# Performance work log

Hardware: AMD Instinct MI355X
Metric: run time of the kernel (lower is better)

Reference implementation:

```python
import jax, jax.numpy as jnp
import numpy as np

N = 50000      # nodes
E = 800000     # edges (avg degree 16)
F_IN = 128
HID = 64
NCLS = 40
K = 2          # num_stacks
T = 2          # num_layers (shared weights)


def setup_inputs() -> dict:
    key = jax.random.key(0)
    ks = jax.random.split(key, 10)
    s = 0.05
    return {
        "x": jax.random.normal(ks[0], (N, F_IN), dtype=jnp.float32),
        "edge_index": jax.random.randint(ks[1], (2, E), 0, N),
        "w1_init": jax.random.normal(ks[2], (K, F_IN, HID), dtype=jnp.float32) * s,
        "w1": jax.random.normal(ks[3], (K, HID, HID), dtype=jnp.float32) * s,
        "v1": jax.random.normal(ks[4], (K, F_IN, HID), dtype=jnp.float32) * s,
        "b1": jax.random.normal(ks[5], (K, HID), dtype=jnp.float32) * s,
        "w2_init": jax.random.normal(ks[6], (K, HID, NCLS), dtype=jnp.float32) * s,
        "w2": jax.random.normal(ks[7], (K, NCLS, NCLS), dtype=jnp.float32) * s,
        "v2": jax.random.normal(ks[8], (K, HID, NCLS), dtype=jnp.float32) * s,
        "b2": jax.random.normal(ks[9], (K, NCLS), dtype=jnp.float32) * s,
    }


def _gcn_norm(src, dst, n):
    # PyG gcn_norm with add_self_loops=False: deg over destination, sym norm
    deg = jax.ops.segment_sum(jnp.ones_like(dst, dtype=jnp.float32), dst, num_segments=n)
    dinv = jnp.where(deg > 0, 1.0 / jnp.sqrt(deg), 0.0)
    return dinv[src] * dinv[dst]  # [E]


def _arma_conv(x, src, dst, norm, n, w_init, w, v, b, act):
    # x: [N, Fin]; w_init: [K, Fin, Fout]; w: [K, Fout, Fout]; v: [K, Fin, Fout]; b: [K, Fout]
    root = jnp.einsum('nf,kfg->kng', x, v)  # [K, N, Fout], dropout=0 -> identity
    out = None
    for t in range(T):
        if t == 0:
            h = jnp.einsum('nf,kfg->kng', x, w_init)
        else:
            h = jnp.einsum('knf,kfg->kng', out, w)
        # sparse neighbor aggregation: out[i] = sum_{(j->i)} norm_e * h[j]
        agg = jax.vmap(
            lambda hk: jax.ops.segment_sum(hk[src] * norm[:, None], dst, num_segments=n)
        )(h)  # [K, N, Fout]
        out = act(agg + root + b[:, None, :])
    return out.mean(axis=0)  # mean over stacks -> [N, Fout]


def reference(x, edge_index, w1_init, w1, v1, b1, w2_init, w2, v2, b2):
    src, dst = edge_index[0], edge_index[1]
    norm = _gcn_norm(src, dst, N)
    h = _arma_conv(x, src, dst, norm, N, w1_init, w1, v1, b1, jax.nn.relu)
    h = jax.nn.relu(h)  # wrapper ReLU; dropout is identity in eval
    o = _arma_conv(h, src, dst, norm, N, w2_init, w2, v2, b2, lambda z: z)
    return jax.nn.log_softmax(o, axis=1)
```

## Files before the change

kernel.cpp:

```cpp
#include <hip/hip_runtime.h>
#include <hip/hip_bf16.h>
#include <math.h>

#define N_NODES 50000
#define F_IN 128
#define HID 64
#define NCLS 40
#define K_STACKS 2
#define SCAN_TILE 1024
#define NBLK_CNT 256

typedef __attribute__((ext_vector_type(8))) short short8;
typedef __attribute__((ext_vector_type(4))) float floatx4;

__device__ __forceinline__ unsigned int f32_to_bf16_bits(float f) {
    unsigned int u = __float_as_uint(f);
    return (u + 0x7fffu + ((u >> 16) & 1u)) >> 16;
}
__device__ __forceinline__ unsigned int pack_bf16x2(float a, float b) {
    return f32_to_bf16_bits(a) | (f32_to_bf16_bits(b) << 16);
}


__global__ __launch_bounds__(256) void count_kernel(const int* __restrict__ dst,
                                                    int* __restrict__ counts, int E) {
    __shared__ int hist[256];
    int blk = blockIdx.x, t = threadIdx.x;
    hist[t] = 0;
    __syncthreads();
    int chunk = (E + NBLK_CNT - 1) / NBLK_CNT;
    int s = blk * chunk, e = min(E, s + chunk);
    for (int i = s + t; i < e; i += 256) atomicAdd(&hist[dst[i] >> 8], 1);
    __syncthreads();
    counts[t * NBLK_CNT + blk] = hist[t];
}

__global__ __launch_bounds__(256) void scan_phase1(const int* __restrict__ in,
                                                   int* __restrict__ blockSums, int n) {
    __shared__ int lds[256];
    int b = blockIdx.x, t = threadIdx.x;
    int base = b * SCAN_TILE + t * 4;
    int s = 0;
    if (base + 3 < n) {
        int4 v = *(const int4*)(in + base);
        s = v.x + v.y + v.z + v.w;
    } else {
#pragma unroll
        for (int i = 0; i < 4; ++i)
            if (base + i < n) s += in[base + i];
    }
    lds[t] = s;
    __syncthreads();
    for (int off = 128; off; off >>= 1) {
        if (t < off) lds[t] += lds[t + off];
        __syncthreads();
    }
    if (t == 0) blockSums[b] = lds[0];
}

__global__ void scan_phase2(int* __restrict__ blockSums, int nb) {
    int t = threadIdx.x;
    int v = (t < nb) ? blockSums[t] : 0;
#pragma unroll
    for (int off = 1; off < 64; off <<= 1) {
        int u = __shfl_up(v, off);
        if (t >= off) v += u;
    }
    if (t < nb) blockSums[t] = v;
}

__global__ __launch_bounds__(256) void scan_phase3_excl(const int* __restrict__ in,
                                                        const int* __restrict__ blockSumsInc,
                                                        int* __restrict__ out, int n) {
    __shared__ int lds[256];
    int b = blockIdx.x, t = threadIdx.x;
    int base = b * SCAN_TILE + t * 4;
    int e[4];
    int s = 0;
#pragma unroll
    for (int i = 0; i < 4; ++i) {
        e[i] = (base + i < n) ? in[base + i] : 0;
        s += e[i];
    }
    lds[t] = s;
    __syncthreads();
    int v = s;
    for (int off = 1; off < 256; off <<= 1) {
        int add = (t >= off) ? lds[t - off] : 0;
        __syncthreads();
        v += add;
        lds[t] = v;
        __syncthreads();
    }
    int run = (t == 0 ? 0 : lds[t - 1]) + (b == 0 ? 0 : blockSumsInc[b - 1]);
#pragma unroll
    for (int i = 0; i < 4; ++i) {
        if (base + i < n) {
            out[base + i] = run;
            run += e[i];
        }
    }
}

__global__ __launch_bounds__(256) void bucket_scatter_kernel(const int* __restrict__ src,
                                                             const int* __restrict__ dst,
                                                             const int* __restrict__ scanned,
                                                             unsigned int* __restrict__ pairs,
                                                             int E) {
    __shared__ int cur[256];
    int blk = blockIdx.x, t = threadIdx.x;
    cur[t] = scanned[t * NBLK_CNT + blk];
    __syncthreads();
    int chunk = (E + NBLK_CNT - 1) / NBLK_CNT;
    int s0 = blk * chunk, e0 = min(E, s0 + chunk);
    for (int i = s0 + t; i < e0; i += 256) {
        int d = dst[i];
        int pos = atomicAdd(&cur[d >> 8], 1);
        pairs[pos] = (unsigned int)src[i] | ((unsigned int)(d & 255) << 16);
    }
}

__global__ __launch_bounds__(256) void csr_build_kernel(const unsigned int* __restrict__ pairs,
                                                        const int* __restrict__ scanned,
                                                        int* __restrict__ row_ptr,
                                                        float* __restrict__ dinv,
                                                        int* __restrict__ col, int N, int E) {
    __shared__ int degl[256], lds[256], curl[256], sb[2];
    int b = blockIdx.x, t = threadIdx.x;
    if (t == 0) {
        sb[0] = scanned[b * NBLK_CNT];
        sb[1] = (b + 1 < 256) ? scanned[(b + 1) * NBLK_CNT] : E;
    }
    degl[t] = 0;
    __syncthreads();
    int bstart = sb[0], bend = sb[1];
    for (int e = bstart + t; e < bend; e += 256) {
        atomicAdd(&degl[(pairs[e] >> 16) & 255], 1);
    }
    __syncthreads();
    int d = degl[t];
    lds[t] = d;
    __syncthreads();
    int v = d;
    for (int off = 1; off < 256; off <<= 1) {
        int add = (t >= off) ? lds[t - off] : 0;
        __syncthreads();
        v += add;
        lds[t] = v;
        __syncthreads();
    }
    int excl = v - d;
    int node = b * 256 + t;
    if (node <= N) row_ptr[node] = bstart + excl;
    if (node < N) dinv[node] = (d > 0) ? (1.0f / sqrtf((float)d)) : 0.0f;
    curl[t] = excl;
    __syncthreads();
    for (int e = bstart + t; e < bend; e += 256) {
        unsigned int p = pairs[e];
        int ln = (p >> 16) & 255;
        int pos = atomicAdd(&curl[ln], 1);
        col[bstart + pos] = (int)(p & 0xffffu);
    }
}

__device__ __forceinline__ void wt_one(const float* __restrict__ in,
                                       unsigned short* __restrict__ out, int li, int C, int F,
                                       int CP) {
    int k = li / (F * CP);
    int r = li - k * F * CP;
    int f = r / CP;
    int c = r - f * CP;
    out[li] = (c < C) ? (unsigned short)f32_to_bf16_bits(in[((size_t)k * C + c) * F + f]) : 0;
}

__global__ void wt_all_kernel(const float* v1, const float* w1i, const float* w1,
                              const float* v2, const float* w2i, const float* w2,
                              unsigned short* v1t, unsigned short* w1it, unsigned short* w1t,
                              unsigned short* v2t, unsigned short* w2it, unsigned short* w2t) {
    int i = blockIdx.x * blockDim.x + threadIdx.x;
    if (i < 16384) wt_one(v1, v1t, i, 128, 64, 128);
    else if (i < 32768) wt_one(w1i, w1it, i - 16384, 128, 64, 128);
    else if (i < 40960) wt_one(w1, w1t, i - 32768, 64, 64, 64);
    else if (i < 46080) wt_one(v2, v2t, i - 40960, 64, 40, 64);
    else if (i < 51200) wt_one(w2i, w2it, i - 46080, 64, 40, 64);
    else if (i < 56320) wt_one(w2, w2t, i - 51200, 40, 40, 64);
}

template <int CINP>
__global__ __launch_bounds__(256) void gemm_mfma(
    const void* __restrict__ A, const unsigned short* __restrict__ Bt,
    void* __restrict__ out, const float* __restrict__ scale, int N, int COUT, int CREAL,
    int a_per_k, int a_bf16, int out_bf16, int do_scale, int out_inter) {
    constexpr int CP8 = CINP / 8;
    constexpr int MS = CP8 - 1;
    constexpr int SH = (CP8 == 16) ? 4 : 3;
    __shared__ __align__(16) unsigned short At[64 * CINP];
    __shared__ __align__(16) unsigned short Bs[64 * CINP];

    const int k = blockIdx.y;
    const int n0 = blockIdx.x * 64;
    const int t = threadIdx.x;
    const size_t abase = a_per_k ? (size_t)k * N * CREAL : (size_t)0;
    const unsigned short* Bk = Bt + (size_t)k * COUT * CINP;

    for (int i = t; i < 64 * CP8; i += 256) {
        int n = i >> SH;
        int c = i & MS;
        uint4 w = make_uint4(0u, 0u, 0u, 0u);
        int gn = n0 + n;
        if (gn < N && c * 8 < CREAL) {
            if (a_bf16) {
                w = *(const uint4*)((const unsigned short*)A + abase + (size_t)gn * CREAL + c * 8);
            } else {
                const float* srcp = (const float*)A + abase + (size_t)gn * CREAL + c * 8;
                float4 f0 = *(const float4*)(srcp);
                float4 f1 = *(const float4*)(srcp + 4);
                w.x = pack_bf16x2(f0.x, f0.y);
                w.y = pack_bf16x2(f0.z, f0.w);
                w.z = pack_bf16x2(f1.x, f1.y);
                w.w = pack_bf16x2(f1.z, f1.w);
            }
        }
        *(uint4*)(At + n * CINP + ((c ^ (n & MS)) << 3)) = w;
    }
    for (int i = t; i < COUT * CP8; i += 256) {
        int f = i >> SH;
        int c = i & MS;
        uint4 w = *(const uint4*)(Bk + f * CINP + c * 8);
        *(uint4*)(Bs + f * CINP + ((c ^ (f & MS)) << 3)) = w;
    }
    __syncthreads();

    const int lane = t & 63;
    const int wv = t >> 6;
    const int quad = lane >> 4;
    const int li = lane & 15;
    const int m0 = wv * 16;

    floatx4 acc[4] = {{0.f, 0.f, 0.f, 0.f}, {0.f, 0.f, 0.f, 0.f},
                      {0.f, 0.f, 0.f, 0.f}, {0.f, 0.f, 0.f, 0.f}};
    const int am = (m0 + li) & MS;
#pragma unroll
    for (int kc = 0; kc < CINP / 32; ++kc) {
        int cc = kc * 4 + quad;
        short8 a = *(const short8*)(At + (m0 + li) * CINP + ((cc ^ am) << 3));
#pragma unroll
        for (int nt = 0; nt < 4; ++nt) {
            if (nt * 16 < COUT) {
                int f = nt * 16 + li;
                short8 b = *(const short8*)(Bs + f * CINP + ((cc ^ (f & MS)) << 3));
                acc[nt] = __builtin_amdgcn_mfma_f32_16x16x32_bf16(a, b, acc[nt], 0, 0, 0);
            }
        }
    }

    float sc[4] = {1.f, 1.f, 1.f, 1.f};
    if (do_scale) {
#pragma unroll
        for (int r = 0; r < 4; ++r) {
            int node = n0 + m0 + quad * 4 + r;
            sc[r] = (node < N) ? scale[node] : 1.f;
        }
    }
#pragma unroll
    for (int nt = 0; nt < 4; ++nt) {
        if (nt * 16 >= COUT) continue;
        int f = nt * 16 + li;
        if (f >= COUT) continue;
#pragma unroll
        for (int r = 0; r < 4; ++r) {
            int node = n0 + m0 + quad * 4 + r;
            if (node < N) {
                size_t o = out_inter ? ((size_t)node * 2 * COUT + (size_t)k * COUT + f)
                                     : (((size_t)k * N + node) * COUT + f);
                float val = acc[nt][r] * sc[r];
                if (out_bf16)
                    ((unsigned short*)out)[o] = (unsigned short)f32_to_bf16_bits(val);
                else
                    ((float*)out)[o] = val;
            }
        }
    }
}

template <int F>
__global__ __launch_bounds__(256) void agg_kernel(
    const unsigned short* __restrict__ h, const int* __restrict__ row_ptr,
    const int* __restrict__ col, const float* __restrict__ dinv,
    const unsigned short* __restrict__ rootb, const float* __restrict__ bias,
    void* __restrict__ out, int N, int do_relu, int out_bf16) {
    constexpr int FH = F / 8;
    constexpr int ROWE = 2 * F;
    int wid = (blockIdx.x * blockDim.x + threadIdx.x) >> 6;
    int lane = threadIdx.x & 63;
    int node = wid;
    if (node >= N) return;
    int e0 = row_ptr[node];
    int deg = row_ptr[node + 1] - e0;
    float dv = dinv[node];
    const int sub = lane >> 4;
    const int fq = lane & 15;
    const int kk = fq >> 3;
    const int fqq = fq & 7;
    const int fqc = (fqq < FH) ? fqq : (FH - 1);
    const int foff = kk * F + fqc * 8;

    float acc[8] = {};
    for (int w0 = 0; w0 < deg; w0 += 64) {
        int mye = w0 + lane;
        int c = (mye < deg) ? col[e0 + mye] : 0;
        int nch = min(deg - w0, 64);
        for (int base = 0; base < nch; base += 16) {
            uint4 v[4];
            float wj[4];
#pragma unroll
            for (int u = 0; u < 4; ++u) {
                int j = base + u * 4 + sub;
                int cj = __shfl(c, j);
                bool ok = (j < nch);
                wj[u] = ok ? 1.f : 0.f;
                int cs = ok ? cj : 0;
                v[u] = *(const uint4*)(h + (size_t)cs * ROWE + foff);
            }
#pragma unroll
            for (int u = 0; u < 4; ++u) {
                const unsigned int uu[4] = {v[u].x, v[u].y, v[u].z, v[u].w};
#pragma unroll
                for (int q = 0; q < 4; ++q) {
                    float lo = __uint_as_float(uu[q] << 16);
                    float hi = __uint_as_float(uu[q] & 0xffff0000u);
                    acc[2 * q] += wj[u] * lo;
                    acc[2 * q + 1] += wj[u] * hi;
                }
            }
        }
    }
#pragma unroll
    for (int m = 16; m < 64; m <<= 1) {
#pragma unroll
        for (int i = 0; i < 8; ++i) acc[i] += __shfl_xor(acc[i], m);
    }
    if (sub == 0 && fqq < FH) {
        size_t o = ((size_t)kk * N + node) * F + fqq * 8;
        uint4 rv = *(const uint4*)(rootb + o);
        const float* bp = bias + kk * F + fqq * 8;
        float4 b0 = *(const float4*)(bp);
        float4 b1 = *(const float4*)(bp + 4);
        const unsigned int ru[4] = {rv.x, rv.y, rv.z, rv.w};
        float r[8];
#pragma unroll
        for (int q = 0; q < 4; ++q) {
            r[2 * q] = __uint_as_float(ru[q] << 16);
            r[2 * q + 1] = __uint_as_float(ru[q] & 0xffff0000u);
        }
        float res[8] = {acc[0] * dv + r[0] + b0.x, acc[1] * dv + r[1] + b0.y,
                        acc[2] * dv + r[2] + b0.z, acc[3] * dv + r[3] + b0.w,
                        acc[4] * dv + r[4] + b1.x, acc[5] * dv + r[5] + b1.y,
                        acc[6] * dv + r[6] + b1.z, acc[7] * dv + r[7] + b1.w};
        if (do_relu) {
#pragma unroll
            for (int i = 0; i < 8; ++i) res[i] = fmaxf(res[i], 0.f);
        }
        if (out_bf16) {
            uint4 w;
            w.x = pack_bf16x2(res[0], res[1]);
            w.y = pack_bf16x2(res[2], res[3]);
            w.z = pack_bf16x2(res[4], res[5]);
            w.w = pack_bf16x2(res[6], res[7]);
            *(uint4*)((unsigned short*)out + o) = w;
        } else {
            *(float4*)((float*)out + o) = make_float4(res[0], res[1], res[2], res[3]);
            *(float4*)((float*)out + o + 4) = make_float4(res[4], res[5], res[6], res[7]);
        }
    }
}

__global__ void mean_relu_kernel(const float* __restrict__ in, float* __restrict__ out,
                                 size_t cnt, size_t stride) {
    size_t i = (size_t)blockIdx.x * blockDim.x + threadIdx.x;
    if (i < cnt) out[i] = fmaxf(0.5f * (in[i] + in[i + stride]), 0.f);
}

__global__ __launch_bounds__(256) void lsm_kernel(const float* __restrict__ g,
                                                  float* __restrict__ out, int N) {
    int wid = (blockIdx.x * blockDim.x + threadIdx.x) >> 6;
    int lane = threadIdx.x & 63;
    if (wid >= N) return;
    float v = -INFINITY;
    if (lane < NCLS)
        v = 0.5f * (g[(size_t)wid * NCLS + lane] + g[((size_t)N + wid) * NCLS + lane]);
    float m = v;
#pragma unroll
    for (int off = 32; off; off >>= 1) m = fmaxf(m, __shfl_xor(m, off));
    float ex = (lane < NCLS) ? expf(v - m) : 0.f;
    float s = ex;
#pragma unroll
    for (int off = 32; off; off >>= 1) s += __shfl_xor(s, off);
    float r = v - m - logf(s);
    if (lane < NCLS) out[(size_t)wid * NCLS + lane] = r;
}


static inline size_t align256(size_t x) { return (x + 255) & ~(size_t)255; }

extern "C" void kernel_launch(void* const* d_in, const int* in_sizes, int n_in,
                              void* d_out, int out_size, void* d_ws, size_t ws_size,
                              hipStream_t stream) {
    const float* x = (const float*)d_in[0];
    const int* ei = (const int*)d_in[1];
    const float* w1_init = (const float*)d_in[2];
    const float* w1 = (const float*)d_in[3];
    const float* v1 = (const float*)d_in[4];
    const float* b1 = (const float*)d_in[5];
    const float* w2_init = (const float*)d_in[6];
    const float* w2 = (const float*)d_in[7];
    const float* v2 = (const float*)d_in[8];
    const float* b2 = (const float*)d_in[9];

    const int N = in_sizes[0] / F_IN;
    const int E = in_sizes[1] / 2;
    const int* src = ei;
    const int* dst = ei + E;

    char* p = (char*)d_ws;
    auto take = [&](size_t bytes) {
        char* r = p;
        p += align256(bytes);
        return r;
    };
    float* dinv = (float*)take((size_t)N * 4);
    int* row_ptr = (int*)take((size_t)(N + 1) * 4);
    int* blockSums = (int*)take(256 * 4);
    int* counts = (int*)take((size_t)256 * NBLK_CNT * 4);
    int* scanned = (int*)take((size_t)256 * NBLK_CNT * 4);
    unsigned int* pairs = (unsigned int*)take((size_t)E * 4);
    int* col = (int*)take((size_t)E * 4);
    unsigned short* v1t = (unsigned short*)take((size_t)2 * 64 * 128 * 2);
    unsigned short* w1it = (unsigned short*)take((size_t)2 * 64 * 128 * 2);
    unsigned short* w1t = (unsigned short*)take((size_t)2 * 64 * 64 * 2);
    unsigned short* v2t = (unsigned short*)take((size_t)2 * 40 * 64 * 2);
    unsigned short* w2it = (unsigned short*)take((size_t)2 * 40 * 64 * 2);
    unsigned short* w2t = (unsigned short*)take((size_t)2 * 40 * 64 * 2);
    unsigned short* rootb = (unsigned short*)take((size_t)K_STACKS * N * HID * 2);
    unsigned short* hb = (unsigned short*)take((size_t)K_STACKS * N * HID * 2);
    unsigned short* hc = (unsigned short*)take((size_t)K_STACKS * N * HID * 2);
    float* bufC = (float*)take((size_t)K_STACKS * N * HID * 4);
    float* h1 = (float*)take((size_t)N * HID * 4);

    const int TB = 256;
    const int nCnt = 256 * NBLK_CNT;
    const int nScanBlocks = nCnt / SCAN_TILE;
    const int nBuckets = (N + 255) / 256;

    count_kernel<<<NBLK_CNT, 256, 0, stream>>>(dst, counts, E);
    scan_phase1<<<nScanBlocks, 256, 0, stream>>>(counts, blockSums, nCnt);
    scan_phase2<<<1, 64, 0, stream>>>(blockSums, nScanBlocks);
    scan_phase3_excl<<<nScanBlocks, 256, 0, stream>>>(counts, blockSums, scanned, nCnt);
    bucket_scatter_kernel<<<NBLK_CNT, 256, 0, stream>>>(src, dst, scanned, pairs, E);
    csr_build_kernel<<<nBuckets, 256, 0, stream>>>(pairs, scanned, row_ptr, dinv, col, N, E);

    wt_all_kernel<<<(56320 + TB - 1) / TB, TB, 0, stream>>>(v1, w1_init, w1, v2, w2_init, w2,
                                                            v1t, w1it, w1t, v2t, w2it, w2t);

    dim3 ggrid((N + 63) / 64, K_STACKS);
    const int agg_blocks = (N + 3) / 4;

    gemm_mfma<128><<<ggrid, 256, 0, stream>>>(x, v1t, rootb, dinv, N, HID, 128, 0, 0, 1, 0, 0);
    gemm_mfma<128><<<ggrid, 256, 0, stream>>>(x, w1it, hb, dinv, N, HID, 128, 0, 0, 1, 1, 1);
    agg_kernel<HID><<<agg_blocks, 256, 0, stream>>>(hb, row_ptr, col, dinv, rootb, b1, hc, N, 1, 1);
    gemm_mfma<64><<<ggrid, 256, 0, stream>>>(hc, w1t, hb, dinv, N, HID, 64, 1, 1, 1, 1, 1);
    agg_kernel<HID><<<agg_blocks, 256, 0, stream>>>(hb, row_ptr, col, dinv, rootb, b1, bufC, N, 1, 0);
    {
        size_t cnt = (size_t)N * HID;
        mean_relu_kernel<<<(cnt + TB - 1) / TB, TB, 0, stream>>>(bufC, h1, cnt, cnt);
    }

    gemm_mfma<64><<<ggrid, 256, 0, stream>>>(h1, v2t, rootb, dinv, N, NCLS, 64, 0, 0, 1, 0, 0);
    gemm_mfma<64><<<ggrid, 256, 0, stream>>>(h1, w2it, hb, dinv, N, NCLS, 64, 0, 0, 1, 1, 1);
    agg_kernel<NCLS><<<agg_blocks, 256, 0, stream>>>(hb, row_ptr, col, dinv, rootb, b2, hc, N, 0, 1);
    gemm_mfma<64><<<ggrid, 256, 0, stream>>>(hc, w2t, hb, dinv, N, NCLS, 40, 1, 1, 1, 1, 1);
    agg_kernel<NCLS><<<agg_blocks, 256, 0, stream>>>(hb, row_ptr, col, dinv, rootb, b2, bufC, N, 0, 0);

    lsm_kernel<<<(N + 3) / 4, 256, 0, stream>>>(bufC, (float*)d_out, N);
}
```

Measured before the change: 339.4 us.

## Process two nodes per wave in aggregation and fuse stack-mean into final agg

The aggregation kernel now maps two nodes per 64-lane wave (32 lanes each) with 8 outstanding row loads per lane instead of 4, which cuts idle lanes for average-degree-16 nodes and raises memory-level parallelism. The last aggregation of each layer now averages the two stacks in registers via a lane shuffle and writes a single mean output. This removes the separate mean_relu kernel and the 2x fp32 intermediate write and read, and simplifies log-softmax to read the pre-averaged tensor. In exchange, the root and bias loads now run on all lanes, including padded ones.

```diff
diff --git a/kernel.cpp b/kernel.cpp
--- a/kernel.cpp
+++ b/kernel.cpp
@@ -288,42 +288,48 @@
     const unsigned short* __restrict__ h, const int* __restrict__ row_ptr,
     const int* __restrict__ col, const float* __restrict__ dinv,
     const unsigned short* __restrict__ rootb, const float* __restrict__ bias,
-    void* __restrict__ out, int N, int do_relu, int out_bf16) {
+    void* __restrict__ out, int N, int do_relu, int mode) {
     constexpr int FH = F / 8;
     constexpr int ROWE = 2 * F;
     int wid = (blockIdx.x * blockDim.x + threadIdx.x) >> 6;
     int lane = threadIdx.x & 63;
-    int node = wid;
-    if (node >= N) return;
-    int e0 = row_ptr[node];
-    int deg = row_ptr[node + 1] - e0;
-    float dv = dinv[node];
-    const int sub = lane >> 4;
-    const int fq = lane & 15;
+    int half = lane >> 5;
+    int l32 = lane & 31;
+    int node = wid * 2 + half;
+    bool valid = node < N;
+    int e0 = 0, deg = 0;
+    float dv = 0.f;
+    if (valid) {
+        e0 = row_ptr[node];
+        deg = row_ptr[node + 1] - e0;
+        dv = dinv[node];
+    }
+    const int sub = l32 >> 4;
+    const int fq = l32 & 15;
     const int kk = fq >> 3;
     const int fqq = fq & 7;
     const int fqc = (fqq < FH) ? fqq : (FH - 1);
     const int foff = kk * F + fqc * 8;
 
     float acc[8] = {};
-    for (int w0 = 0; w0 < deg; w0 += 64) {
-        int mye = w0 + lane;
+    for (int w0 = 0; w0 < deg; w0 += 32) {
+        int mye = w0 + l32;
         int c = (mye < deg) ? col[e0 + mye] : 0;
-        int nch = min(deg - w0, 64);
+        int nch = min(deg - w0, 32);
         for (int base = 0; base < nch; base += 16) {
-            uint4 v[4];
-            float wj[4];
-#pragma unroll
-            for (int u = 0; u < 4; ++u) {
-                int j = base + u * 4 + sub;
-                int cj = __shfl(c, j);
+            uint4 v[8];
+            float wj[8];
+#pragma unroll
+            for (int u = 0; u < 8; ++u) {
+                int j = base + u * 2 + sub;
+                int cj = __shfl(c, (half << 5) | (j & 31));
                 bool ok = (j < nch);
                 wj[u] = ok ? 1.f : 0.f;
                 int cs = ok ? cj : 0;
                 v[u] = *(const uint4*)(h + (size_t)cs * ROWE + foff);
             }
 #pragma unroll
-            for (int u = 0; u < 4; ++u) {
+            for (int u = 0; u < 8; ++u) {
                 const unsigned int uu[4] = {v[u].x, v[u].y, v[u].z, v[u].w};
 #pragma unroll
                 for (int q = 0; q < 4; ++q) {
@@ -336,49 +342,48 @@
         }
     }
 #pragma unroll
-    for (int m = 16; m < 64; m <<= 1) {
-#pragma unroll
-        for (int i = 0; i < 8; ++i) acc[i] += __shfl_xor(acc[i], m);
-    }
-    if (sub == 0 && fqq < FH) {
-        size_t o = ((size_t)kk * N + node) * F + fqq * 8;
-        uint4 rv = *(const uint4*)(rootb + o);
-        const float* bp = bias + kk * F + fqq * 8;
-        float4 b0 = *(const float4*)(bp);
-        float4 b1 = *(const float4*)(bp + 4);
-        const unsigned int ru[4] = {rv.x, rv.y, rv.z, rv.w};
-        float r[8];
-#pragma unroll
-        for (int q = 0; q < 4; ++q) {
-            r[2 * q] = __uint_as_float(ru[q] << 16);
-            r[2 * q + 1] = __uint_as_float(ru[q] & 0xffff0000u);
-        }
-        float res[8] = {acc[0] * dv + r[0] + b0.x, acc[1] * dv + r[1] + b0.y,
-                        acc[2] * dv + r[2] + b0.z, acc[3] * dv + r[3] + b0.w,
-                        acc[4] * dv + r[4] + b1.x, acc[5] * dv + r[5] + b1.y,
-                        acc[6] * dv + r[6] + b1.z, acc[7] * dv + r[7] + b1.w};
-        if (do_relu) {
-#pragma unroll
-            for (int i = 0; i < 8; ++i) res[i] = fmaxf(res[i], 0.f);
-        }
-        if (out_bf16) {
+    for (int i = 0; i < 8; ++i) acc[i] += __shfl_xor(acc[i], 16);
+
+    size_t oc = ((size_t)kk * N + (valid ? node : 0)) * F + fqc * 8;
+    uint4 rv = *(const uint4*)(rootb + oc);
+    const float* bp = bias + kk * F + fqc * 8;
+    float4 b0 = *(const float4*)(bp);
+    float4 b1 = *(const float4*)(bp + 4);
+    const unsigned int ru[4] = {rv.x, rv.y, rv.z, rv.w};
+    float res[8];
+#pragma unroll
+    for (int q = 0; q < 4; ++q) {
+        float rlo = __uint_as_float(ru[q] << 16);
+        float rhi = __uint_as_float(ru[q] & 0xffff0000u);
+        float blo = (q < 2) ? ((q == 0) ? b0.x : b0.z) : ((q == 2) ? b1.x : b1.z);
+        float bhi = (q < 2) ? ((q == 0) ? b0.y : b0.w) : ((q == 2) ? b1.y : b1.w);
+        res[2 * q] = acc[2 * q] * dv + rlo + blo;
+        res[2 * q + 1] = acc[2 * q + 1] * dv + rhi + bhi;
+    }
+    if (do_relu) {
+#pragma unroll
+        for (int i = 0; i < 8; ++i) res[i] = fmaxf(res[i], 0.f);
+    }
+    if (mode == 0) {
+        if (sub == 0 && fqq < FH && valid) {
+            size_t o = ((size_t)kk * N + node) * F + fqq * 8;
             uint4 w;
             w.x = pack_bf16x2(res[0], res[1]);
             w.y = pack_bf16x2(res[2], res[3]);
             w.z = pack_bf16x2(res[4], res[5]);
             w.w = pack_bf16x2(res[6], res[7]);
             *(uint4*)((unsigned short*)out + o) = w;
-        } else {
-            *(float4*)((float*)out + o) = make_float4(res[0], res[1], res[2], res[3]);
-            *(float4*)((float*)out + o + 4) = make_float4(res[4], res[5], res[6], res[7]);
-        }
-    }
-}
-
-__global__ void mean_relu_kernel(const float* __restrict__ in, float* __restrict__ out,
-                                 size_t cnt, size_t stride) {
-    size_t i = (size_t)blockIdx.x * blockDim.x + threadIdx.x;
-    if (i < cnt) out[i] = fmaxf(0.5f * (in[i] + in[i + stride]), 0.f);
+        }
+    } else {
+        float mres[8];
+#pragma unroll
+        for (int i = 0; i < 8; ++i) mres[i] = 0.5f * (res[i] + __shfl_xor(res[i], 8));
+        if (sub == 0 && kk == 0 && fqq < FH && valid) {
+            size_t o = (size_t)node * F + fqq * 8;
+            *(float4*)((float*)out + o) = make_float4(mres[0], mres[1], mres[2], mres[3]);
+            *(float4*)((float*)out + o + 4) = make_float4(mres[4], mres[5], mres[6], mres[7]);
+        }
+    }
 }
 
 __global__ __launch_bounds__(256) void lsm_kernel(const float* __restrict__ g,
@@ -386,9 +391,7 @@
     int wid = (blockIdx.x * blockDim.x + threadIdx.x) >> 6;
     int lane = threadIdx.x & 63;
     if (wid >= N) return;
-    float v = -INFINITY;
-    if (lane < NCLS)
-        v = 0.5f * (g[(size_t)wid * NCLS + lane] + g[((size_t)N + wid) * NCLS + lane]);
+    float v = (lane < NCLS) ? g[(size_t)wid * NCLS + lane] : -INFINITY;
     float m = v;
 #pragma unroll
     for (int off = 32; off; off >>= 1) m = fmaxf(m, __shfl_xor(m, off));
@@ -444,8 +447,8 @@
     unsigned short* rootb = (unsigned short*)take((size_t)K_STACKS * N * HID * 2);
     unsigned short* hb = (unsigned short*)take((size_t)K_STACKS * N * HID * 2);
     unsigned short* hc = (unsigned short*)take((size_t)K_STACKS * N * HID * 2);
-    float* bufC = (float*)take((size_t)K_STACKS * N * HID * 4);
     float* h1 = (float*)take((size_t)N * HID * 4);
+    float* gmean = (float*)take((size_t)N * NCLS * 4);
 
     const int TB = 256;
     const int nCnt = 256 * NBLK_CNT;
@@ -463,23 +466,19 @@
                                                             v1t, w1it, w1t, v2t, w2it, w2t);
 
     dim3 ggrid((N + 63) / 64, K_STACKS);
-    const int agg_blocks = (N + 3) / 4;
+    const int agg_blocks = ((N + 1) / 2 + 3) / 4;
 
     gemm_mfma<128><<<ggrid, 256, 0, stream>>>(x, v1t, rootb, dinv, N, HID, 128, 0, 0, 1, 0, 0);
     gemm_mfma<128><<<ggrid, 256, 0, stream>>>(x, w1it, hb, dinv, N, HID, 128, 0, 0, 1, 1, 1);
-    agg_kernel<HID><<<agg_blocks, 256, 0, stream>>>(hb, row_ptr, col, dinv, rootb, b1, hc, N, 1, 1);
+    agg_kernel<HID><<<agg_blocks, 256, 0, stream>>>(hb, row_ptr, col, dinv, rootb, b1, hc, N, 1, 0);
     gemm_mfma<64><<<ggrid, 256, 0, stream>>>(hc, w1t, hb, dinv, N, HID, 64, 1, 1, 1, 1, 1);
-    agg_kernel<HID><<<agg_blocks, 256, 0, stream>>>(hb, row_ptr, col, dinv, rootb, b1, bufC, N, 1, 0);
-    {
-        size_t cnt = (size_t)N * HID;
-        mean_relu_kernel<<<(cnt + TB - 1) / TB, TB, 0, stream>>>(bufC, h1, cnt, cnt);
-    }
+    agg_kernel<HID><<<agg_blocks, 256, 0, stream>>>(hb, row_ptr, col, dinv, rootb, b1, h1, N, 1, 1);
 
     gemm_mfma<64><<<ggrid, 256, 0, stream>>>(h1, v2t, rootb, dinv, N, NCLS, 64, 0, 0, 1, 0, 0);
     gemm_mfma<64><<<ggrid, 256, 0, stream>>>(h1, w2it, hb, dinv, N, NCLS, 64, 0, 0, 1, 1, 1);
-    agg_kernel<NCLS><<<agg_blocks, 256, 0, stream>>>(hb, row_ptr, col, dinv, rootb, b2, hc, N, 0, 1);
+    agg_kernel<NCLS><<<agg_blocks, 256, 0, stream>>>(hb, row_ptr, col, dinv, rootb, b2, hc, N, 0, 0);
     gemm_mfma<64><<<ggrid, 256, 0, stream>>>(hc, w2t, hb, dinv, N, NCLS, 40, 1, 1, 1, 1, 1);
-    agg_kernel<NCLS><<<agg_blocks, 256, 0, stream>>>(hb, row_ptr, col, dinv, rootb, b2, bufC, N, 0, 0);
-
-    lsm_kernel<<<(N + 3) / 4, 256, 0, stream>>>(bufC, (float*)d_out, N);
-}
+    agg_kernel<NCLS><<<agg_blocks, 256, 0, stream>>>(hb, row_ptr, col, dinv, rootb, b2, gmean, N, 0, 1);
+
+    lsm_kernel<<<(N + 3) / 4, 256, 0, stream>>>(gmean, (float*)d_out, N);
+}
```

After: 339.7 us. About the same (+0.1%).
